# Optimization experiments

Measured on AMD Instinct MI355X. Metric: run time of the kernel, lower is better.

Reference implementation:

```python
import jax, jax.numpy as jnp
import numpy as np

N_NODES = 100000
N_EDGES = 1600000
N_GRAPHS = 512
HID = 192
EPS = 1e-5


def setup_inputs() -> dict:
    key = jax.random.key(0)
    ks = jax.random.split(key, 16)
    x = jax.random.normal(ks[0], (N_NODES, 1), dtype=jnp.float32)
    edge_index = jax.random.randint(ks[1], (2, N_EDGES), 0, N_NODES, dtype=jnp.int64)
    batch = jnp.sort(jax.random.randint(ks[2], (N_NODES,), 0, N_GRAPHS, dtype=jnp.int64))
    def lin(k, fi, fo):
        # torch nn.Linear default init: U(-1/sqrt(fi), 1/sqrt(fi))
        b = 1.0 / np.sqrt(fi)
        return jax.random.uniform(k, (fi, fo), jnp.float32, -b, b)
    return {
        "x": x, "edge_index": edge_index, "batch": batch,
        "W1": lin(ks[3], 1, HID), "b1": jnp.zeros((HID,), jnp.float32),
        "g1": jnp.ones((HID,), jnp.float32), "be1": jnp.zeros((HID,), jnp.float32), "a1": jnp.ones((HID,), jnp.float32),
        "W2": lin(ks[4], HID, HID), "b2": jnp.zeros((HID,), jnp.float32),
        "g2": jnp.ones((HID,), jnp.float32), "be2": jnp.zeros((HID,), jnp.float32), "a2": jnp.ones((HID,), jnp.float32),
        "Wc1": lin(ks[5], HID, HID // 2), "bc1": jax.random.uniform(ks[6], (HID // 2,), jnp.float32, -1/np.sqrt(HID), 1/np.sqrt(HID)),
        "Wc2": lin(ks[7], HID // 2, 4), "bc2": jax.random.uniform(ks[8], (4,), jnp.float32, -1/np.sqrt(HID // 2), 1/np.sqrt(HID // 2)),
    }


def gcn_conv(x, W, b, row, col, n):
    # PyG GCNConv: h = xW; add self-loops; norm = d^-1/2[src] * d^-1/2[dst]; scatter-add to dst; + bias
    h = x @ W
    sl = jnp.arange(n, dtype=row.dtype)
    r = jnp.concatenate([row, sl])
    c = jnp.concatenate([col, sl])
    deg = jax.ops.segment_sum(jnp.ones_like(c, dtype=h.dtype), c, num_segments=n)
    dinv = jnp.where(deg > 0, jax.lax.rsqrt(deg), 0.0)
    norm = dinv[r] * dinv[c]                      # [E+N]
    msg = h[r] * norm[:, None]                    # [E+N, HID] dominant gather
    return jax.ops.segment_sum(msg, c, num_segments=n) + b


def graph_norm(x, batch, gamma, beta, alpha, g):
    cnt = jax.ops.segment_sum(jnp.ones((x.shape[0],), x.dtype), batch, num_segments=g)
    cnt = jnp.maximum(cnt, 1.0)[:, None]
    mean = jax.ops.segment_sum(x, batch, num_segments=g) / cnt
    out = x - alpha * mean[batch]
    var = jax.ops.segment_sum(out * out, batch, num_segments=g) / cnt
    out = out * jax.lax.rsqrt(var + EPS)[batch]
    return gamma * out + beta


def reference(x, edge_index, batch, W1, b1, g1, be1, a1, W2, b2, g2, be2, a2, Wc1, bc1, Wc2, bc2):
    n = x.shape[0]
    row, col = edge_index[0], edge_index[1]
    h = gcn_conv(x, W1, b1, row, col, n)
    h = jax.nn.relu(graph_norm(h, batch, g1, be1, a1, N_GRAPHS))
    h = gcn_conv(h, W2, b2, row, col, n)
    h = jax.nn.relu(graph_norm(h, batch, g2, be2, a2, N_GRAPHS))
    # global mean pool (dropout is identity in eval mode)
    cnt = jnp.maximum(jax.ops.segment_sum(jnp.ones((n,), h.dtype), batch, num_segments=N_GRAPHS), 1.0)
    pooled = jax.ops.segment_sum(h, batch, num_segments=N_GRAPHS) / cnt[:, None]
    z = jax.nn.relu(pooled @ Wc1 + bc1)
    return z @ Wc2 + bc2
```

## Files before the change

### kernel.cpp

```cpp
#include <hip/hip_runtime.h>
#include <hip/hip_bf16.h>
#include <hip/hip_fp16.h>

#define N_NODES 100000
#define N_PAD 100032
#define N_EDGES 1600000
#define N_GRAPHS 512
#define HID 192
#define EPSV 1e-5f

using f16x8 = __attribute__((ext_vector_type(8))) _Float16;
using f16x4 = __attribute__((ext_vector_type(4))) _Float16;
using f32x4 = __attribute__((ext_vector_type(4))) float;

__global__ void k_count(const int* __restrict__ col, int* __restrict__ cnt) {
    int e = blockIdx.x * blockDim.x + threadIdx.x;
    if (e < N_EDGES) atomicAdd(&cnt[col[e]], 1);
}

__global__ void k_misc(const float* __restrict__ W2, _Float16* __restrict__ W2h,
                       const int* __restrict__ batch, int* __restrict__ gstart) {
    int id = blockIdx.x * blockDim.x + threadIdx.x;
    if (id < HID * HID) W2h[id] = (_Float16)W2[id];
    int g = id - HID * HID;
    if (g >= 0 && g <= N_GRAPHS) {
        if (g == N_GRAPHS) { gstart[g] = N_NODES; return; }
        int lo = 0, hi = N_NODES;
        while (lo < hi) { int mid = (lo + hi) >> 1; if (batch[mid] < g) lo = mid + 1; else hi = mid; }
        gstart[g] = lo;
    }
}

__global__ void k_scan_partial(const int* __restrict__ cnt, int* __restrict__ bsum) {
    __shared__ int sd[256];
    int base = blockIdx.x * 1024;
    int t = threadIdx.x;
    int s = 0;
    for (int j = 0; j < 4; ++j) {
        int i = base + j * 256 + t;
        if (i < N_NODES) s += cnt[i];
    }
    sd[t] = s; __syncthreads();
    for (int off = 128; off > 0; off >>= 1) {
        if (t < off) sd[t] += sd[t + off];
        __syncthreads();
    }
    if (t == 0) bsum[blockIdx.x] = sd[0];
}

__global__ void k_scan_final(const int* __restrict__ cnt, const int* __restrict__ bsum,
                             int nb, int* __restrict__ row_ptr, int* __restrict__ cursor,
                             float* __restrict__ dinv, const float* __restrict__ x,
                             float* __restrict__ xp) {
    __shared__ int sd[256];
    __shared__ int s_off;
    int bid = blockIdx.x;
    int t = threadIdx.x;
    int part = 0;
    for (int i = t; i < bid; i += 256) part += bsum[i];
    sd[t] = part; __syncthreads();
    for (int off = 128; off > 0; off >>= 1) {
        if (t < off) sd[t] += sd[t + off];
        __syncthreads();
    }
    if (t == 0) s_off = sd[0];
    __syncthreads();
    int base = bid * 1024;
    int idx0 = base + t * 4;
    int c[4]; int tot = 0;
    for (int j = 0; j < 4; ++j) {
        int i = idx0 + j;
        c[j] = (i < N_NODES) ? cnt[i] : 0;
        tot += c[j];
    }
    sd[t] = tot; __syncthreads();
    for (int off = 1; off < 256; off <<= 1) {
        int v = (t >= off) ? sd[t - off] : 0;
        __syncthreads();
        sd[t] += v;
        __syncthreads();
    }
    int excl = sd[t] - tot + s_off;
    for (int j = 0; j < 4; ++j) {
        int i = idx0 + j;
        if (i < N_NODES) {
            row_ptr[i] = excl;
            cursor[i] = excl;
            float dv = rsqrtf((float)(c[j] + 1));
            dinv[i] = dv;
            xp[i] = x[i] * dv;
            excl += c[j];
        }
    }
    if (bid == nb - 1 && t == 255) row_ptr[N_NODES] = excl;
}

#define FILL_WIN 8
#define FILL_RANGE (N_NODES / FILL_WIN)
#define EPR ((N_EDGES + 255) / 256)
__global__ void __launch_bounds__(256) k_fill(const int* __restrict__ row,
                                              const int* __restrict__ col,
                                              int* __restrict__ cursor,
                                              int* __restrict__ csr_src) {
    int w = blockIdx.x & 7;
    int rank = blockIdx.x >> 3;
    int lo = w * FILL_RANGE;
    int hi = (w == FILL_WIN - 1) ? N_NODES : lo + FILL_RANGE;
    int e0 = rank * EPR;
    int e1 = min(e0 + EPR, N_EDGES);
    for (int e = e0 + threadIdx.x; e < e1; e += 256) {
        int c = col[e];
        if (c >= lo && c < hi) {
            int pos = atomicAdd(&cursor[c], 1);
            csr_src[pos] = row[e];
        }
    }
}

__global__ void k_layer1(const float* __restrict__ x, const float* __restrict__ xp,
                         const int* __restrict__ batch,
                         const int* __restrict__ row_ptr, const int* __restrict__ csr_src,
                         const float* __restrict__ dinv, float4* __restrict__ node_info) {
    int v = blockIdx.x * blockDim.x + threadIdx.x;
    if (v >= N_NODES) return;
    int e0 = row_ptr[v], e1 = row_ptr[v + 1];
    float acc = 0.f;
    for (int base = e0; base < e1; base += 16) {
        int src[16]; float xv[16];
#pragma unroll
        for (int j = 0; j < 16; ++j) { int e = base + j; src[j] = csr_src[(e < e1) ? e : e0]; }
#pragma unroll
        for (int j = 0; j < 16; ++j) { xv[j] = xp[src[j]]; }
#pragma unroll
        for (int j = 0; j < 16; ++j) { acc += (base + j < e1) ? xv[j] : 0.f; }
    }
    float dv = dinv[v];
    float u = dv * acc + x[v] * dv * dv;
    node_info[v] = make_float4(u, dv, __int_as_float((int)batch[v]), 0.f);
}

__global__ void __launch_bounds__(192) k_stats_ab(const float4* __restrict__ node_info,
                                                  const int* __restrict__ gstart,
                                                  const float* __restrict__ W1, const float* __restrict__ b1,
                                                  const float* __restrict__ g1, const float* __restrict__ be1,
                                                  const float* __restrict__ a1,
                                                  float* __restrict__ A, float* __restrict__ B) {
    __shared__ float sd[192], sd2[192];
    int g = blockIdx.x, t = threadIdx.x;
    int i0 = gstart[g], i1 = gstart[g + 1];
    float s = 0.f, s2 = 0.f;
    for (int i = i0 + t; i < i1; i += 192) { float u = node_info[i].x; s += u; s2 += u * u; }
    sd[t] = s; sd2[t] = s2; __syncthreads();
    for (int off = 96; off >= 3; off >>= 1) {
        if (t < off) { sd[t] += sd[t + off]; sd2[t] += sd2[t + off]; }
        __syncthreads();
    }
    float sum_u = sd[0] + sd[1] + sd[2];
    float sum_u2 = sd2[0] + sd2[1] + sd2[2];
    float cntf = fmaxf((float)(i1 - i0), 1.f);
    float m = sum_u / cntf;
    float es2 = sum_u2 / cntf;
    int f = t;
    float w = W1[f], bb = b1[f], al = a1[f];
    float c2 = bb * (1.f - al);
    float d = al * m;
    float eud2 = es2 - 2.f * d * m + d * d;
    float var = w * w * eud2 + 2.f * w * c2 * (m - d) + c2 * c2;
    float rs = rsqrtf(var + EPSV);
    float gam = g1[f];
    A[g * HID + f] = gam * rs * w;
    B[g * HID + f] = gam * rs * (c2 - w * d) + be1[f];
}

__global__ void __launch_bounds__(256) k_x1(const float4* __restrict__ node_info,
                                            const float* __restrict__ A,
                                            const float* __restrict__ B,
                                            _Float16* __restrict__ X1p) {
    int wid = threadIdx.x >> 6;
    int lane = threadIdx.x & 63;
    int v = blockIdx.x * 4 + wid;
    if (v >= N_NODES) return;
    float4 ni = node_info[v];
    float u = ni.x, dv = ni.y;
    int g = __float_as_int(ni.z);
    int c4 = (lane < 48 ? lane : 47) * 4;
    float4 Av = *(const float4*)(A + g * HID + c4);
    float4 Bv = *(const float4*)(B + g * HID + c4);
    f16x4 o;
    o[0] = (_Float16)(fmaxf(fmaf(Av.x, u, Bv.x), 0.f) * dv);
    o[1] = (_Float16)(fmaxf(fmaf(Av.y, u, Bv.y), 0.f) * dv);
    o[2] = (_Float16)(fmaxf(fmaf(Av.z, u, Bv.z), 0.f) * dv);
    o[3] = (_Float16)(fmaxf(fmaf(Av.w, u, Bv.w), 0.f) * dv);
    if (lane < 48) *(f16x4*)(X1p + (size_t)v * HID + c4) = o;
}

#define CH 8
__global__ void __launch_bounds__(256) k_conv2(const _Float16* __restrict__ X1p,
                                               const float* __restrict__ dinv,
                                               const int* __restrict__ row_ptr,
                                               const int* __restrict__ csr_src,
                                               _Float16* __restrict__ aggh) {
    int wid = threadIdx.x >> 6;
    int lane = threadIdx.x & 63;
    int v = blockIdx.x * 4 + wid;
    if (v >= N_NODES) return;
    unsigned c8 = (unsigned)(lane < 48 ? lane : 47) * 8u;
    const char* Xb = (const char*)X1p;
    float dv = dinv[v];
    f16x4 sv = *(const f16x4*)(Xb + (unsigned)v * (HID * 2) + c8);
    float a0 = (float)sv[0], a1 = (float)sv[1], a2 = (float)sv[2], a3 = (float)sv[3];
    int e0 = row_ptr[v], e1 = row_ptr[v + 1];
    for (int b = e0; b < e1; b += CH) {
        unsigned off[CH]; float wgt[CH];
#pragma unroll
        for (int j = 0; j < CH; ++j) {
            int e = b + j;
            off[j] = (unsigned)csr_src[(e < e1) ? e : e0] * (unsigned)(HID * 2) + c8;
            wgt[j] = (e < e1) ? 1.f : 0.f;
        }
        f16x4 rv[CH];
#pragma unroll
        for (int j = 0; j < CH; ++j)
            rv[j] = *(const f16x4*)(Xb + off[j]);
#pragma unroll
        for (int j = 0; j < CH; ++j) {
            a0 = fmaf(wgt[j], (float)rv[j][0], a0);
            a1 = fmaf(wgt[j], (float)rv[j][1], a1);
            a2 = fmaf(wgt[j], (float)rv[j][2], a2);
            a3 = fmaf(wgt[j], (float)rv[j][3], a3);
        }
    }
    if (lane < 48) {
        f16x4 o;
        o[0] = (_Float16)(a0 * dv);
        o[1] = (_Float16)(a1 * dv);
        o[2] = (_Float16)(a2 * dv);
        o[3] = (_Float16)(a3 * dv);
        *(f16x4*)((char*)aggh + (unsigned)v * (HID * 2) + c8) = o;
    }
}

#define BM 64
__global__ void __launch_bounds__(256) k_gemm(const _Float16* __restrict__ A,
                                              const _Float16* __restrict__ W,
                                              const float* __restrict__ b2,
                                              _Float16* __restrict__ H) {
    __shared__ _Float16 a_lds[BM * HID];
    int t = threadIdx.x;
    int wid = t >> 6, lane = t & 63;
    int row0 = blockIdx.x * BM;
    const char* Ablk = (const char*)(A + (size_t)row0 * HID);
#pragma unroll
    for (int it = 0; it < 6; ++it) {
        int bo = (it * 256 + t) * 16;
        int r = bo / 384;
        int swz = bo ^ ((r & 7) << 4);
        *(float4*)((char*)a_lds + swz) = *(const float4*)(Ablk + bo);
    }
    int n0 = wid * 48;
    int bn = n0 + (lane & 15);
    int bk0 = (lane >> 4) << 3;
    f16x8 bfr[6][3];
#pragma unroll
    for (int kc = 0; kc < 6; ++kc)
#pragma unroll
        for (int nt = 0; nt < 3; ++nt) {
            const _Float16* src = W + (size_t)(kc * 32 + bk0) * HID + bn + nt * 16;
            f16x8 v;
#pragma unroll
            for (int j = 0; j < 8; ++j) v[j] = src[(size_t)j * HID];
            bfr[kc][nt] = v;
        }
    __syncthreads();
    f32x4 acc[4][3];
#pragma unroll
    for (int mt = 0; mt < 4; ++mt)
#pragma unroll
        for (int nt = 0; nt < 3; ++nt) acc[mt][nt] = (f32x4){0.f, 0.f, 0.f, 0.f};
    int ar = lane & 15;
#pragma unroll
    for (int mt = 0; mt < 4; ++mt) {
        int r = mt * 16 + ar;
        int rbase = r * 384;
        int sw = (r & 7) << 4;
#pragma unroll
        for (int kc = 0; kc < 6; ++kc) {
            int bo = (rbase + (kc * 32 + bk0) * 2) ^ sw;
            f16x8 a = *(const f16x8*)((const char*)a_lds + bo);
            acc[mt][0] = __builtin_amdgcn_mfma_f32_16x16x32_f16(a, bfr[kc][0], acc[mt][0], 0, 0, 0);
            acc[mt][1] = __builtin_amdgcn_mfma_f32_16x16x32_f16(a, bfr[kc][1], acc[mt][1], 0, 0, 0);
            acc[mt][2] = __builtin_amdgcn_mfma_f32_16x16x32_f16(a, bfr[kc][2], acc[mt][2], 0, 0, 0);
        }
    }
    int cn = lane & 15;
    int rb = (lane >> 4) * 4;
    float bias[3];
#pragma unroll
    for (int nt = 0; nt < 3; ++nt) bias[nt] = b2[n0 + nt * 16 + cn];
#pragma unroll
    for (int mt = 0; mt < 4; ++mt)
#pragma unroll
        for (int nt = 0; nt < 3; ++nt) {
            int col = n0 + nt * 16 + cn;
#pragma unroll
            for (int r = 0; r < 4; ++r) {
                int grow = row0 + mt * 16 + rb + r;
                if (grow < N_NODES)
                    H[(size_t)grow * HID + col] = (_Float16)(acc[mt][nt][r] + bias[nt]);
            }
        }
}

__global__ void __launch_bounds__(192) k_stats2(const _Float16* __restrict__ h,
                                                const int* __restrict__ batch,
                                                float* __restrict__ sums,
                                                float* __restrict__ sumsq) {
    int f = threadIdx.x;
    int r0 = blockIdx.x * 64;
    int r1 = min(r0 + 64, N_NODES);
    int g = batch[r0];
    float s = 0.f, s2 = 0.f;
    int i = r0;
    for (; i + 4 <= r1; i += 4) {
        int g0 = batch[i], g3 = batch[i + 3];
        float v0 = (float)h[(size_t)(i + 0) * HID + f];
        float v1 = (float)h[(size_t)(i + 1) * HID + f];
        float v2 = (float)h[(size_t)(i + 2) * HID + f];
        float v3 = (float)h[(size_t)(i + 3) * HID + f];
        if (g0 == g && g3 == g) {
            s += v0 + v1 + v2; s += v3;
            s2 += v0 * v0 + v1 * v1; s2 += v2 * v2 + v3 * v3;
        } else {
            float vv[4] = {v0, v1, v2, v3};
            for (int j = 0; j < 4; ++j) {
                int gi = batch[i + j];
                if (gi != g) {
                    atomicAdd(&sums[g * HID + f], s);
                    atomicAdd(&sumsq[g * HID + f], s2);
                    s = 0.f; s2 = 0.f; g = gi;
                }
                s += vv[j]; s2 += vv[j] * vv[j];
            }
        }
    }
    for (; i < r1; ++i) {
        int gi = batch[i];
        float v = (float)h[(size_t)i * HID + f];
        if (gi != g) {
            atomicAdd(&sums[g * HID + f], s);
            atomicAdd(&sumsq[g * HID + f], s2);
            s = 0.f; s2 = 0.f; g = gi;
        }
        s += v; s2 += v * v;
    }
    atomicAdd(&sums[g * HID + f], s);
    atomicAdd(&sumsq[g * HID + f], s2);
}

__global__ void k_cd(const float* __restrict__ sums, const float* __restrict__ sumsq,
                     const int* __restrict__ gstart,
                     const float* __restrict__ g2, const float* __restrict__ be2,
                     const float* __restrict__ a2,
                     float* __restrict__ C, float* __restrict__ D) {
    int id = blockIdx.x * blockDim.x + threadIdx.x;
    if (id >= N_GRAPHS * HID) return;
    int g = id / HID, f = id % HID;
    float cntf = fmaxf((float)(gstart[g + 1] - gstart[g]), 1.f);
    float mh = sums[id] / cntf;
    float msq = sumsq[id] / cntf;
    float al = a2[f];
    float var = msq - 2.f * al * mh * mh + al * al * mh * mh;
    float Cv = g2[f] * rsqrtf(var + EPSV);
    C[id] = Cv;
    D[id] = be2[f] - Cv * al * mh;
}

__global__ void __launch_bounds__(192) k_pool(const _Float16* __restrict__ h,
                                              const int* __restrict__ batch,
                                              const float* __restrict__ C,
                                              const float* __restrict__ D,
                                              float* __restrict__ pooled) {
    int f = threadIdx.x;
    int r0 = blockIdx.x * 64;
    int r1 = min(r0 + 64, N_NODES);
    int g = batch[r0];
    float Cg = C[g * HID + f], Dg = D[g * HID + f];
    float s = 0.f;
    int i = r0;
    for (; i + 4 <= r1; i += 4) {
        int g0 = batch[i], g3 = batch[i + 3];
        float v0 = (float)h[(size_t)(i + 0) * HID + f];
        float v1 = (float)h[(size_t)(i + 1) * HID + f];
        float v2 = (float)h[(size_t)(i + 2) * HID + f];
        float v3 = (float)h[(size_t)(i + 3) * HID + f];
        if (g0 == g && g3 == g) {
            s += fmaxf(fmaf(Cg, v0, Dg), 0.f) + fmaxf(fmaf(Cg, v1, Dg), 0.f);
            s += fmaxf(fmaf(Cg, v2, Dg), 0.f) + fmaxf(fmaf(Cg, v3, Dg), 0.f);
        } else {
            float vv[4] = {v0, v1, v2, v3};
            for (int j = 0; j < 4; ++j) {
                int gi = batch[i + j];
                if (gi != g) {
                    atomicAdd(&pooled[g * HID + f], s);
                    s = 0.f; g = gi;
                    Cg = C[g * HID + f]; Dg = D[g * HID + f];
                }
                s += fmaxf(fmaf(Cg, vv[j], Dg), 0.f);
            }
        }
    }
    for (; i < r1; ++i) {
        int gi = batch[i];
        float v = (float)h[(size_t)i * HID + f];
        if (gi != g) {
            atomicAdd(&pooled[g * HID + f], s);
            s = 0.f; g = gi;
            Cg = C[g * HID + f]; Dg = D[g * HID + f];
        }
        s += fmaxf(fmaf(Cg, v, Dg), 0.f);
    }
    atomicAdd(&pooled[g * HID + f], s);
}

__global__ void __launch_bounds__(128) k_mlp(const float* __restrict__ pooled,
                                             const int* __restrict__ gstart,
                                             const float* __restrict__ Wc1,
                                             const float* __restrict__ bc1,
                                             const float* __restrict__ Wc2,
                                             const float* __restrict__ bc2,
                                             float* __restrict__ out) {
    __shared__ float p[HID];
    __shared__ float z[96];
    int g = blockIdx.x, t = threadIdx.x;
    float inv = 1.f / fmaxf((float)(gstart[g + 1] - gstart[g]), 1.f);
    for (int i = t; i < HID; i += 128) p[i] = pooled[g * HID + i] * inv;
    __syncthreads();
    if (t < 96) {
        float acc = bc1[t];
        for (int k = 0; k < HID; ++k) acc += p[k] * Wc1[k * 96 + t];
        z[t] = fmaxf(acc, 0.f);
    }
    __syncthreads();
    if (t < 4) {
        float acc = bc2[t];
        for (int j = 0; j < 96; ++j) acc += z[j] * Wc2[j * 4 + t];
        out[g * 4 + t] = acc;
    }
}

extern "C" void kernel_launch(void* const* d_in, const int* in_sizes, int n_in,
                              void* d_out, int out_size, void* d_ws, size_t ws_size,
                              hipStream_t stream) {
    const float* x   = (const float*)d_in[0];
    const int* eidx  = (const int*)d_in[1];
    const int* batch = (const int*)d_in[2];
    const float* W1  = (const float*)d_in[3];
    const float* b1  = (const float*)d_in[4];
    const float* g1  = (const float*)d_in[5];
    const float* be1 = (const float*)d_in[6];
    const float* a1  = (const float*)d_in[7];
    const float* W2  = (const float*)d_in[8];
    const float* b2  = (const float*)d_in[9];
    const float* g2  = (const float*)d_in[10];
    const float* be2 = (const float*)d_in[11];
    const float* a2  = (const float*)d_in[12];
    const float* Wc1 = (const float*)d_in[13];
    const float* bc1 = (const float*)d_in[14];
    const float* Wc2 = (const float*)d_in[15];
    const float* bc2 = (const float*)d_in[16];
    const int* row = eidx;
    const int* col = eidx + N_EDGES;
    float* out = (float*)d_out;

    char* ws = (char*)d_ws;
    size_t off = 0;
    auto alloc = [&](size_t bytes) -> char* {
        char* p = ws + off;
        off = (off + bytes + 255) & ~(size_t)255;
        return p;
    };
    int*   cnt     = (int*)  alloc(N_NODES * 4);
    float* sums2   = (float*)alloc(N_GRAPHS * HID * 4);
    float* sumsq2  = (float*)alloc(N_GRAPHS * HID * 4);
    float* pooled  = (float*)alloc(N_GRAPHS * HID * 4);
    size_t zbytes  = off;
    int*   bsum    = (int*)  alloc(128 * 4);
    int*   row_ptr = (int*)  alloc((N_NODES + 1) * 4);
    int*   cursor  = (int*)  alloc(N_NODES * 4);
    int*   csr_src = (int*)  alloc(N_EDGES * 4);
    float* dinv    = (float*)alloc(N_NODES * 4);
    float* xp      = (float*)alloc(N_NODES * 4);
    float4* node_info = (float4*)alloc((size_t)N_NODES * 16);
    float* Atab    = (float*)alloc(N_GRAPHS * HID * 4);
    float* Btab    = (float*)alloc(N_GRAPHS * HID * 4);
    float* Ctab    = (float*)alloc(N_GRAPHS * HID * 4);
    float* Dtab    = (float*)alloc(N_GRAPHS * HID * 4);
    int*   gstart  = (int*)  alloc((N_GRAPHS + 1) * 4);
    _Float16* X1p  = (_Float16*)alloc((size_t)N_NODES * HID * 2);
    _Float16* aggh = (_Float16*)alloc((size_t)N_PAD * HID * 2);
    _Float16* h2   = (_Float16*)alloc((size_t)N_NODES * HID * 2);
    _Float16* W2h  = (_Float16*)alloc((size_t)HID * HID * 2);

    hipMemsetAsync(ws, 0, zbytes, stream);
    k_misc<<<(HID * HID + N_GRAPHS + 1 + 255) / 256, 256, 0, stream>>>(W2, W2h, batch, gstart);
    k_count<<<(N_EDGES + 255) / 256, 256, 0, stream>>>(col, cnt);
    int PB = (N_NODES + 1023) / 1024;
    k_scan_partial<<<PB, 256, 0, stream>>>(cnt, bsum);
    k_scan_final<<<PB, 256, 0, stream>>>(cnt, bsum, PB, row_ptr, cursor, dinv, x, xp);
    k_fill<<<2048, 256, 0, stream>>>(row, col, cursor, csr_src);
    k_layer1<<<(N_NODES + 255) / 256, 256, 0, stream>>>(x, xp, batch, row_ptr, csr_src, dinv, node_info);
    k_stats_ab<<<N_GRAPHS, 192, 0, stream>>>(node_info, gstart, W1, b1, g1, be1, a1, Atab, Btab);
    k_x1<<<(N_NODES + 3) / 4, 256, 0, stream>>>(node_info, Atab, Btab, X1p);
    k_conv2<<<(N_NODES + 3) / 4, 256, 0, stream>>>(X1p, dinv, row_ptr, csr_src, aggh);
    k_gemm<<<(N_NODES + BM - 1) / BM, 256, 0, stream>>>(aggh, W2h, b2, h2);
    int SB = (N_NODES + 63) / 64;
    k_stats2<<<SB, 192, 0, stream>>>(h2, batch, sums2, sumsq2);
    k_cd<<<(N_GRAPHS * HID + 255) / 256, 256, 0, stream>>>(sums2, sumsq2, gstart,
                                                           g2, be2, a2, Ctab, Dtab);
    k_pool<<<SB, 192, 0, stream>>>(h2, batch, Ctab, Dtab, pooled);
    k_mlp<<<N_GRAPHS, 128, 0, stream>>>(pooled, gstart, Wc1, bc1, Wc2, bc2, out);
}
```

Baseline: 348.0 us.

## Fuse layer-1 aggregation into CSR fill and stats into GEMM epilogue

The separate layer-1 gather kernel is removed. Each edge's xp[src] is now atomically accumulated into an interleaved cursor/accumulator array during the CSR fill. GraphNorm-2 sum and sum-of-squares are computed in the GEMM epilogue, assuming each 64-row block spans at most two graphs, so the k_stats2 pass over h2 is gone. The C/D table kernel is folded into k_pool. This cuts three kernel launches and one full re-read of h2, at the cost of extra float atomics in k_fill, nondeterministic summation order, and a correctness dependence on the two-graphs-per-block assumption.

```diff
diff --git a/kernel.cpp b/kernel.cpp
--- a/kernel.cpp
+++ b/kernel.cpp
@@ -49,7 +49,7 @@
 }
 
 __global__ void k_scan_final(const int* __restrict__ cnt, const int* __restrict__ bsum,
-                             int nb, int* __restrict__ row_ptr, int* __restrict__ cursor,
+                             int nb, int* __restrict__ row_ptr, int* __restrict__ cur_acc,
                              float* __restrict__ dinv, const float* __restrict__ x,
                              float* __restrict__ xp) {
     __shared__ int sd[256];
@@ -85,7 +85,8 @@
         int i = idx0 + j;
         if (i < N_NODES) {
             row_ptr[i] = excl;
-            cursor[i] = excl;
+            cur_acc[2 * i] = excl;
+            cur_acc[2 * i + 1] = 0;
             float dv = rsqrtf((float)(c[j] + 1));
             dinv[i] = dv;
             xp[i] = x[i] * dv;
@@ -100,7 +101,8 @@
 #define EPR ((N_EDGES + 255) / 256)
 __global__ void __launch_bounds__(256) k_fill(const int* __restrict__ row,
                                               const int* __restrict__ col,
-                                              int* __restrict__ cursor,
+                                              const float* __restrict__ xp,
+                                              int* __restrict__ cur_acc,
                                               int* __restrict__ csr_src) {
     int w = blockIdx.x & 7;
     int rank = blockIdx.x >> 3;
@@ -111,35 +113,17 @@
     for (int e = e0 + threadIdx.x; e < e1; e += 256) {
         int c = col[e];
         if (c >= lo && c < hi) {
-            int pos = atomicAdd(&cursor[c], 1);
-            csr_src[pos] = row[e];
-        }
-    }
-}
-
-__global__ void k_layer1(const float* __restrict__ x, const float* __restrict__ xp,
-                         const int* __restrict__ batch,
-                         const int* __restrict__ row_ptr, const int* __restrict__ csr_src,
-                         const float* __restrict__ dinv, float4* __restrict__ node_info) {
-    int v = blockIdx.x * blockDim.x + threadIdx.x;
-    if (v >= N_NODES) return;
-    int e0 = row_ptr[v], e1 = row_ptr[v + 1];
-    float acc = 0.f;
-    for (int base = e0; base < e1; base += 16) {
-        int src[16]; float xv[16];
-#pragma unroll
-        for (int j = 0; j < 16; ++j) { int e = base + j; src[j] = csr_src[(e < e1) ? e : e0]; }
-#pragma unroll
-        for (int j = 0; j < 16; ++j) { xv[j] = xp[src[j]]; }
-#pragma unroll
-        for (int j = 0; j < 16; ++j) { acc += (base + j < e1) ? xv[j] : 0.f; }
-    }
-    float dv = dinv[v];
-    float u = dv * acc + x[v] * dv * dv;
-    node_info[v] = make_float4(u, dv, __int_as_float((int)batch[v]), 0.f);
-}
-
-__global__ void __launch_bounds__(192) k_stats_ab(const float4* __restrict__ node_info,
+            int r = row[e];
+            int pos = atomicAdd(&cur_acc[2 * c], 1);
+            atomicAdd((float*)&cur_acc[2 * c + 1], xp[r]);
+            csr_src[pos] = r;
+        }
+    }
+}
+
+__global__ void __launch_bounds__(192) k_stats_ab(const int* __restrict__ cur_acc,
+                                                  const float* __restrict__ x,
+                                                  const float* __restrict__ dinv,
                                                   const int* __restrict__ gstart,
                                                   const float* __restrict__ W1, const float* __restrict__ b1,
                                                   const float* __restrict__ g1, const float* __restrict__ be1,
@@ -148,8 +132,13 @@
     __shared__ float sd[192], sd2[192];
     int g = blockIdx.x, t = threadIdx.x;
     int i0 = gstart[g], i1 = gstart[g + 1];
+    const float* ca = (const float*)cur_acc;
     float s = 0.f, s2 = 0.f;
-    for (int i = i0 + t; i < i1; i += 192) { float u = node_info[i].x; s += u; s2 += u * u; }
+    for (int i = i0 + t; i < i1; i += 192) {
+        float dv = dinv[i];
+        float u = dv * (ca[2 * i + 1] + x[i] * dv);
+        s += u; s2 += u * u;
+    }
     sd[t] = s; sd2[t] = s2; __syncthreads();
     for (int off = 96; off >= 3; off >>= 1) {
         if (t < off) { sd[t] += sd[t + off]; sd2[t] += sd2[t + off]; }
@@ -172,7 +161,10 @@
     B[g * HID + f] = gam * rs * (c2 - w * d) + be1[f];
 }
 
-__global__ void __launch_bounds__(256) k_x1(const float4* __restrict__ node_info,
+__global__ void __launch_bounds__(256) k_x1(const int* __restrict__ cur_acc,
+                                            const float* __restrict__ x,
+                                            const float* __restrict__ dinv,
+                                            const int* __restrict__ batch,
                                             const float* __restrict__ A,
                                             const float* __restrict__ B,
                                             _Float16* __restrict__ X1p) {
@@ -180,9 +172,9 @@
     int lane = threadIdx.x & 63;
     int v = blockIdx.x * 4 + wid;
     if (v >= N_NODES) return;
-    float4 ni = node_info[v];
-    float u = ni.x, dv = ni.y;
-    int g = __float_as_int(ni.z);
+    float dv = dinv[v];
+    float u = dv * (((const float*)cur_acc)[2 * v + 1] + x[v] * dv);
+    int g = batch[v];
     int c4 = (lane < 48 ? lane : 47) * 4;
     float4 Av = *(const float4*)(A + g * HID + c4);
     float4 Bv = *(const float4*)(B + g * HID + c4);
@@ -244,11 +236,16 @@
 __global__ void __launch_bounds__(256) k_gemm(const _Float16* __restrict__ A,
                                               const _Float16* __restrict__ W,
                                               const float* __restrict__ b2,
-                                              _Float16* __restrict__ H) {
+                                              const int* __restrict__ batch,
+                                              _Float16* __restrict__ H,
+                                              float* __restrict__ sums,
+                                              float* __restrict__ sumsq) {
     __shared__ _Float16 a_lds[BM * HID];
+    __shared__ int bb[BM];
     int t = threadIdx.x;
     int wid = t >> 6, lane = t & 63;
     int row0 = blockIdx.x * BM;
+    if (t < BM) { int gr = row0 + t; bb[t] = (gr < N_NODES) ? batch[gr] : -1; }
     const char* Ablk = (const char*)(A + (size_t)row0 * HID);
 #pragma unroll
     for (int it = 0; it < 6; ++it) {
@@ -297,94 +294,74 @@
     float bias[3];
 #pragma unroll
     for (int nt = 0; nt < 3; ++nt) bias[nt] = b2[n0 + nt * 16 + cn];
+    int gA = bb[0];
+    int lastv = min(BM, N_NODES - row0) - 1;
+    int gB = bb[lastv];
+    float sA[3] = {0.f,0.f,0.f}, qA[3] = {0.f,0.f,0.f};
+    float sB[3] = {0.f,0.f,0.f}, qB[3] = {0.f,0.f,0.f};
 #pragma unroll
     for (int mt = 0; mt < 4; ++mt)
 #pragma unroll
+        for (int r = 0; r < 4; ++r) {
+            int ridx = mt * 16 + rb + r;
+            int grow = row0 + ridx;
+            if (grow < N_NODES) {
+                int gi = bb[ridx];
+                _Float16* o = H + (size_t)grow * HID;
+#pragma unroll
+                for (int nt = 0; nt < 3; ++nt) {
+                    float val = acc[mt][nt][r] + bias[nt];
+                    o[n0 + nt * 16 + cn] = (_Float16)val;
+                    if (gi == gA) { sA[nt] += val; qA[nt] += val * val; }
+                    else          { sB[nt] += val; qB[nt] += val * val; }
+                }
+            }
+        }
+#pragma unroll
+    for (int nt = 0; nt < 3; ++nt) {
+        sA[nt] += __shfl_xor(sA[nt], 16); sA[nt] += __shfl_xor(sA[nt], 32);
+        qA[nt] += __shfl_xor(qA[nt], 16); qA[nt] += __shfl_xor(qA[nt], 32);
+        sB[nt] += __shfl_xor(sB[nt], 16); sB[nt] += __shfl_xor(sB[nt], 32);
+        qB[nt] += __shfl_xor(qB[nt], 16); qB[nt] += __shfl_xor(qB[nt], 32);
+    }
+    if (lane < 16) {
+#pragma unroll
         for (int nt = 0; nt < 3; ++nt) {
-            int col = n0 + nt * 16 + cn;
-#pragma unroll
-            for (int r = 0; r < 4; ++r) {
-                int grow = row0 + mt * 16 + rb + r;
-                if (grow < N_NODES)
-                    H[(size_t)grow * HID + col] = (_Float16)(acc[mt][nt][r] + bias[nt]);
+            int colf = n0 + nt * 16 + cn;
+            atomicAdd(&sums[gA * HID + colf], sA[nt]);
+            atomicAdd(&sumsq[gA * HID + colf], qA[nt]);
+            if (gB != gA) {
+                atomicAdd(&sums[gB * HID + colf], sB[nt]);
+                atomicAdd(&sumsq[gB * HID + colf], qB[nt]);
             }
         }
-}
-
-__global__ void __launch_bounds__(192) k_stats2(const _Float16* __restrict__ h,
-                                                const int* __restrict__ batch,
-                                                float* __restrict__ sums,
-                                                float* __restrict__ sumsq) {
-    int f = threadIdx.x;
-    int r0 = blockIdx.x * 64;
-    int r1 = min(r0 + 64, N_NODES);
-    int g = batch[r0];
-    float s = 0.f, s2 = 0.f;
-    int i = r0;
-    for (; i + 4 <= r1; i += 4) {
-        int g0 = batch[i], g3 = batch[i + 3];
-        float v0 = (float)h[(size_t)(i + 0) * HID + f];
-        float v1 = (float)h[(size_t)(i + 1) * HID + f];
-        float v2 = (float)h[(size_t)(i + 2) * HID + f];
-        float v3 = (float)h[(size_t)(i + 3) * HID + f];
-        if (g0 == g && g3 == g) {
-            s += v0 + v1 + v2; s += v3;
-            s2 += v0 * v0 + v1 * v1; s2 += v2 * v2 + v3 * v3;
-        } else {
-            float vv[4] = {v0, v1, v2, v3};
-            for (int j = 0; j < 4; ++j) {
-                int gi = batch[i + j];
-                if (gi != g) {
-                    atomicAdd(&sums[g * HID + f], s);
-                    atomicAdd(&sumsq[g * HID + f], s2);
-                    s = 0.f; s2 = 0.f; g = gi;
-                }
-                s += vv[j]; s2 += vv[j] * vv[j];
-            }
-        }
-    }
-    for (; i < r1; ++i) {
-        int gi = batch[i];
-        float v = (float)h[(size_t)i * HID + f];
-        if (gi != g) {
-            atomicAdd(&sums[g * HID + f], s);
-            atomicAdd(&sumsq[g * HID + f], s2);
-            s = 0.f; s2 = 0.f; g = gi;
-        }
-        s += v; s2 += v * v;
-    }
-    atomicAdd(&sums[g * HID + f], s);
-    atomicAdd(&sumsq[g * HID + f], s2);
-}
-
-__global__ void k_cd(const float* __restrict__ sums, const float* __restrict__ sumsq,
-                     const int* __restrict__ gstart,
-                     const float* __restrict__ g2, const float* __restrict__ be2,
-                     const float* __restrict__ a2,
-                     float* __restrict__ C, float* __restrict__ D) {
-    int id = blockIdx.x * blockDim.x + threadIdx.x;
-    if (id >= N_GRAPHS * HID) return;
-    int g = id / HID, f = id % HID;
-    float cntf = fmaxf((float)(gstart[g + 1] - gstart[g]), 1.f);
-    float mh = sums[id] / cntf;
-    float msq = sumsq[id] / cntf;
-    float al = a2[f];
-    float var = msq - 2.f * al * mh * mh + al * al * mh * mh;
-    float Cv = g2[f] * rsqrtf(var + EPSV);
-    C[id] = Cv;
-    D[id] = be2[f] - Cv * al * mh;
+    }
 }
 
 __global__ void __launch_bounds__(192) k_pool(const _Float16* __restrict__ h,
                                               const int* __restrict__ batch,
-                                              const float* __restrict__ C,
-                                              const float* __restrict__ D,
+                                              const int* __restrict__ gstart,
+                                              const float* __restrict__ sums,
+                                              const float* __restrict__ sumsq,
+                                              const float* __restrict__ g2,
+                                              const float* __restrict__ be2,
+                                              const float* __restrict__ a2,
                                               float* __restrict__ pooled) {
     int f = threadIdx.x;
     int r0 = blockIdx.x * 64;
     int r1 = min(r0 + 64, N_NODES);
+    float al = a2[f], gam = g2[f], bet = be2[f];
     int g = batch[r0];
-    float Cg = C[g * HID + f], Dg = D[g * HID + f];
+    float Cg, Dg;
+    auto cd = [&](int gg) {
+        float cntf = fmaxf((float)(gstart[gg + 1] - gstart[gg]), 1.f);
+        float mh = sums[gg * HID + f] / cntf;
+        float msq = sumsq[gg * HID + f] / cntf;
+        float var = msq - 2.f * al * mh * mh + al * al * mh * mh;
+        Cg = gam * rsqrtf(var + EPSV);
+        Dg = bet - Cg * al * mh;
+    };
+    cd(g);
     float s = 0.f;
     int i = r0;
     for (; i + 4 <= r1; i += 4) {
@@ -402,8 +379,7 @@
                 int gi = batch[i + j];
                 if (gi != g) {
                     atomicAdd(&pooled[g * HID + f], s);
-                    s = 0.f; g = gi;
-                    Cg = C[g * HID + f]; Dg = D[g * HID + f];
+                    s = 0.f; g = gi; cd(g);
                 }
                 s += fmaxf(fmaf(Cg, vv[j], Dg), 0.f);
             }
@@ -414,8 +390,7 @@
         float v = (float)h[(size_t)i * HID + f];
         if (gi != g) {
             atomicAdd(&pooled[g * HID + f], s);
-            s = 0.f; g = gi;
-            Cg = C[g * HID + f]; Dg = D[g * HID + f];
+            s = 0.f; g = gi; cd(g);
         }
         s += fmaxf(fmaf(Cg, v, Dg), 0.f);
     }
@@ -486,15 +461,12 @@
     size_t zbytes  = off;
     int*   bsum    = (int*)  alloc(128 * 4);
     int*   row_ptr = (int*)  alloc((N_NODES + 1) * 4);
-    int*   cursor  = (int*)  alloc(N_NODES * 4);
+    int*   cur_acc = (int*)  alloc((size_t)N_NODES * 8);
     int*   csr_src = (int*)  alloc(N_EDGES * 4);
     float* dinv    = (float*)alloc(N_NODES * 4);
     float* xp      = (float*)alloc(N_NODES * 4);
-    float4* node_info = (float4*)alloc((size_t)N_NODES * 16);
     float* Atab    = (float*)alloc(N_GRAPHS * HID * 4);
     float* Btab    = (float*)alloc(N_GRAPHS * HID * 4);
-    float* Ctab    = (float*)alloc(N_GRAPHS * HID * 4);
-    float* Dtab    = (float*)alloc(N_GRAPHS * HID * 4);
     int*   gstart  = (int*)  alloc((N_GRAPHS + 1) * 4);
     _Float16* X1p  = (_Float16*)alloc((size_t)N_NODES * HID * 2);
     _Float16* aggh = (_Float16*)alloc((size_t)N_PAD * HID * 2);
@@ -506,17 +478,13 @@
     k_count<<<(N_EDGES + 255) / 256, 256, 0, stream>>>(col, cnt);
     int PB = (N_NODES + 1023) / 1024;
     k_scan_partial<<<PB, 256, 0, stream>>>(cnt, bsum);
-    k_scan_final<<<PB, 256, 0, stream>>>(cnt, bsum, PB, row_ptr, cursor, dinv, x, xp);
-    k_fill<<<2048, 256, 0, stream>>>(row, col, cursor, csr_src);
-    k_layer1<<<(N_NODES + 255) / 256, 256, 0, stream>>>(x, xp, batch, row_ptr, csr_src, dinv, node_info);
-    k_stats_ab<<<N_GRAPHS, 192, 0, stream>>>(node_info, gstart, W1, b1, g1, be1, a1, Atab, Btab);
-    k_x1<<<(N_NODES + 3) / 4, 256, 0, stream>>>(node_info, Atab, Btab, X1p);
+    k_scan_final<<<PB, 256, 0, stream>>>(cnt, bsum, PB, row_ptr, cur_acc, dinv, x, xp);
+    k_fill<<<2048, 256, 0, stream>>>(row, col, xp, cur_acc, csr_src);
+    k_stats_ab<<<N_GRAPHS, 192, 0, stream>>>(cur_acc, x, dinv, gstart, W1, b1, g1, be1, a1, Atab, Btab);
+    k_x1<<<(N_NODES + 3) / 4, 256, 0, stream>>>(cur_acc, x, dinv, batch, Atab, Btab, X1p);
     k_conv2<<<(N_NODES + 3) / 4, 256, 0, stream>>>(X1p, dinv, row_ptr, csr_src, aggh);
-    k_gemm<<<(N_NODES + BM - 1) / BM, 256, 0, stream>>>(aggh, W2h, b2, h2);
+    k_gemm<<<(N_NODES + BM - 1) / BM, 256, 0, stream>>>(aggh, W2h, b2, batch, h2, sums2, sumsq2);
     int SB = (N_NODES + 63) / 64;
-    k_stats2<<<SB, 192, 0, stream>>>(h2, batch, sums2, sumsq2);
-    k_cd<<<(N_GRAPHS * HID + 255) / 256, 256, 0, stream>>>(sums2, sumsq2, gstart,
-                                                           g2, be2, a2, Ctab, Dtab);
-    k_pool<<<SB, 192, 0, stream>>>(h2, batch, Ctab, Dtab, pooled);
+    k_pool<<<SB, 192, 0, stream>>>(h2, batch, gstart, sums2, sumsq2, g2, be2, a2, pooled);
     k_mlp<<<N_GRAPHS, 128, 0, stream>>>(pooled, gstart, Wc1, bc1, Wc2, bc2, out);
 }
```

Result: slower. 400.6 us (+15.1%).
